# Kernel optimization log

Measured on AMD Instinct MI355X. Metric: run time of the kernel, lower is better.

The kernel has to match this reference:

```python
import jax, jax.numpy as jnp
import numpy as np

PAD = 1
K = 3  # kernel_size


def conv2d(x, w, b):
    y = jax.lax.conv_general_dilated(
        x, w, window_strides=(1, 1), padding=((PAD, PAD), (PAD, PAD)),
        dimension_numbers=("NCHW", "OIHW", "NCHW"))
    return y + b[None, :, None, None]


def deform_conv2d(x, offset, weight, bias):
    # torchvision.ops.deform_conv2d semantics (stride=1, dilation=1, 1 offset group)
    B, C, H, W = x.shape
    O = weight.shape[0]
    K2 = K * K
    off = offset.reshape(B, K2, 2, H, W)  # [...,0]=dy, [...,1]=dx
    ky, kx = jnp.meshgrid(jnp.arange(K), jnp.arange(K), indexing="ij")
    ky = ky.reshape(K2).astype(x.dtype)
    kx = kx.reshape(K2).astype(x.dtype)
    hh = jnp.arange(H, dtype=x.dtype)
    ww = jnp.arange(W, dtype=x.dtype)
    # sampling coords, shape [B, K2, H, W]
    py = off[:, :, 0] + ky[None, :, None, None] + hh[None, None, :, None] - PAD
    px = off[:, :, 1] + kx[None, :, None, None] + ww[None, None, None, :] - PAD

    y0 = jnp.floor(py)
    x0 = jnp.floor(px)
    wy = (py - y0)[:, None]  # [B,1,K2,H,W]
    wx = (px - x0)[:, None]

    xf = x.reshape(B, C, H * W)

    def gather(iy, ix):
        valid = (iy >= 0) & (iy < H) & (ix >= 0) & (ix < W)
        iyc = jnp.clip(iy, 0, H - 1).astype(jnp.int32)
        ixc = jnp.clip(ix, 0, W - 1).astype(jnp.int32)
        idx = (iyc * W + ixc).reshape(B, 1, K2 * H * W)
        v = jnp.take_along_axis(xf, idx, axis=2).reshape(B, C, K2, H, W)
        return v * valid.reshape(B, 1, K2, H, W).astype(x.dtype)

    v00 = gather(y0, x0)
    v01 = gather(y0, x0 + 1)
    v10 = gather(y0 + 1, x0)
    v11 = gather(y0 + 1, x0 + 1)
    sampled = (v00 * (1 - wy) * (1 - wx) + v01 * (1 - wy) * wx
               + v10 * wy * (1 - wx) + v11 * wy * wx)  # [B,C,K2,H,W]
    out = jnp.einsum("bckhw,ock->bohw", sampled, weight.reshape(O, C, K2))
    return out + bias[None, :, None, None]


def setup_inputs() -> dict:
    key = jax.random.key(0)
    k1, k2, k3, k4, k5 = jax.random.split(key, 5)
    B, C, H, W = 4, 64, 192, 192
    O = 64
    x = jax.random.normal(k1, (B, C, H, W), dtype=jnp.float32)
    w_off = jax.random.normal(k2, (2 * K * K, C, K, K), dtype=jnp.float32) * 0.05
    b_off = jnp.zeros((2 * K * K,), dtype=jnp.float32)
    w_conv = jax.random.normal(k3, (O, C, K, K), dtype=jnp.float32) * (1.0 / np.sqrt(C * K * K))
    b_conv = jax.random.normal(k4, (O,), dtype=jnp.float32) * 0.01
    return {"x": x, "w_off": w_off, "b_off": b_off, "w_conv": w_conv, "b_conv": b_conv}


def reference(x, w_off, b_off, w_conv, b_conv):
    offset = conv2d(x, w_off, b_off)
    y = deform_conv2d(x, offset, w_conv, b_conv)
    return conv2d(y, w_conv, b_conv)  # module reuses self.conv on deform output
```

## Files before the change

kernel.cpp:

```cpp
#include <hip/hip_runtime.h>

constexpr int B = 4;
constexpr int C = 64;
constexpr int O = 64;
constexpr int OOFF = 18;
constexpr int H = 192;
constexpr int W = 192;

typedef __attribute__((ext_vector_type(8))) short short8;
typedef __attribute__((ext_vector_type(4))) float float4v;
typedef __attribute__((ext_vector_type(2))) float f32x2;
typedef __attribute__((ext_vector_type(2))) uint u32x2;
typedef __attribute__((ext_vector_type(2))) __bf16 bf16x2;

__device__ inline ushort f2bf(float f) {
  return __builtin_bit_cast(ushort, (__bf16)f);
}
__device__ inline uint pk2bf(float lo, float hi) {
  bf16x2 v;
  v.x = (__bf16)lo;
  v.y = (__bf16)hi;
  return __builtin_bit_cast(uint, v);
}
__device__ inline f32x2 upk(uint u) {
  u32x2 t;
  t.x = u << 16;
  t.y = u & 0xffff0000u;
  return __builtin_bit_cast(f32x2, t);
}

__global__ __launch_bounds__(256) void k_pre(const float* __restrict__ x,
                                             ushort* __restrict__ xtb,
                                             const float* __restrict__ w_conv,
                                             ushort* __restrict__ wBf,
                                             const float* __restrict__ w_off,
                                             ushort* __restrict__ wOf) {
  __shared__ float tile[64][17];
  const int bid = blockIdx.x;
  const int tid = threadIdx.x;
  if (bid < 9216) {
    const int w0 = (bid % 12) * 16;
    const int h = (bid / 12) % 192;
    const int b = bid / 2304;
    const int wl = tid & 15;
    const int c0 = tid >> 4;
#pragma unroll
    for (int r = 0; r < 4; ++r) {
      const int c = c0 + r * 16;
      tile[c][wl] = x[(((size_t)b * C + c) * H + h) * W + w0 + wl];
    }
    __syncthreads();
    const int c = tid & 63;
    const int qq = tid >> 6;
#pragma unroll
    for (int r = 0; r < 4; ++r) {
      const int wq = qq + r * 4;
      xtb[(((size_t)b * H + h) * W + w0 + wq) * C + c] = f2bf(tile[c][wq]);
    }
  } else if (bid < 9360) {
    const int i = (bid - 9216) * 256 + tid;
    const int j = i & 7;
    const int lane = (i >> 3) & 63;
    const int nt = (i >> 9) & 3;
    const int kstep = (i >> 11) & 1;
    const int kk = i >> 12;
    const int n = nt + 4 * (lane & 15);
    const int c = kstep * 32 + ((lane >> 4) & 3) * 8 + j;
    wBf[i] = f2bf(w_conv[((size_t)n * C + c) * 9 + kk]);
  } else {
    const int i = (bid - 9360) * 256 + tid;
    const int j = i & 7;
    const int lane = (i >> 3) & 63;
    const int nt = (i >> 9) & 1;
    const int ks = (i >> 10) & 1;
    const int kk = i >> 11;
    const int n = nt * 16 + (lane & 15);
    const int c = ks * 32 + ((lane >> 4) & 3) * 8 + j;
    wOf[i] = (n < OOFF) ? f2bf(w_off[((size_t)n * C + c) * 9 + kk]) : (ushort)0;
  }
}

__global__ __launch_bounds__(256) void k_fused(
    const ushort* __restrict__ xtb, const ushort* __restrict__ wOf,
    const float* __restrict__ b_off, const ushort* __restrict__ wBf,
    const float* __restrict__ b_conv, ushort* __restrict__ yt) {
  __shared__ ushort sA[4][2][64][8];
  __shared__ __align__(16) float offBuf[4][16][20];

  const int bid = blockIdx.x;
  const int xcd = bid & 7;
  const int s = bid >> 3;
  const int b = xcd >> 1;
  const int half = xcd & 1;
  const int th = half * 12 + s / 24;
  const int tw = s % 24;
  const int h0 = th * 8, w0 = tw * 8;

  const int tid = threadIdx.x;
  const int wave = tid >> 6, lane = tid & 63;
  const int col = lane & 15, quad = lane >> 4;
  const int p = tid >> 2, qtr = tid & 3;
  const int pl = p & 15;
  const int prow = p >> 3, pcol = p & 7;
  const int h = h0 + prow, w = w0 + pcol;
  const int ks_w = qtr >> 1;
  const int q2 = (qtr & 1) * 2;

  {
    float4v oacc[2];
#pragma unroll
    for (int nt = 0; nt < 2; ++nt) oacc[nt] = (float4v){0.f, 0.f, 0.f, 0.f};

    short8 obfr[2][2][2];
    short8 oafr[2][2];

    auto oload = [&](int kk, int pb) {
      const int ky = kk / 3, kx = kk % 3;
      const int hh = h0 + 2 * wave + (col >> 3) + ky - 1;
      const int ww = w0 + (col & 7) + kx - 1;
      const bool ok = ((unsigned)hh < (unsigned)H) && ((unsigned)ww < (unsigned)W);
      const int hhc = min(max(hh, 0), H - 1);
      const int wwc = min(max(ww, 0), W - 1);
      const ushort* pa = xtb + (((size_t)b * H + hhc) * W + wwc) * C + quad * 8;
#pragma unroll
      for (int ks = 0; ks < 2; ++ks) {
        short8 v = (short8)0;
        if (ok) v = *(const short8*)(pa + ks * 32);
        oafr[pb][ks] = v;
#pragma unroll
        for (int nt = 0; nt < 2; ++nt)
          obfr[pb][ks][nt] = *(const short8*)&wOf[((((size_t)kk * 2 + ks) * 2 + nt) * 64 + lane) * 8];
      }
    };

    oload(0, 0);
#pragma unroll
    for (int kk = 0; kk < 9; ++kk) {
      const int pb = kk & 1;
      if (kk < 8) oload(kk + 1, pb ^ 1);
#pragma unroll
      for (int ks = 0; ks < 2; ++ks)
#pragma unroll
        for (int nt = 0; nt < 2; ++nt)
          oacc[nt] = __builtin_amdgcn_mfma_f32_16x16x32_bf16(oafr[pb][ks], obfr[pb][ks][nt],
                                                             oacc[nt], 0, 0, 0);
    }

#pragma unroll
    for (int nt = 0; nt < 2; ++nt) {
      const int oc = nt * 16 + col;
      if (oc < OOFF) {
        const float bias = b_off[oc];
#pragma unroll
        for (int r = 0; r < 4; ++r)
          offBuf[wave][quad * 4 + r][oc] = oacc[nt][r] + bias;
      }
    }
  }

  const ushort* xb = xtb + (size_t)b * H * W * C + qtr * 16;

  uint4 G[2][8];
  float4 aw[2];

  auto issue = [&](int kk, int buf) {
    const float2 ov = *(const float2*)&offBuf[wave][pl][2 * kk];
    const float dy = ov.x, dx = ov.y;
    const int ky = kk / 3, kx = kk % 3;
    const float pyf = dy + (float)(ky + h - 1);
    const float pxf = dx + (float)(kx + w - 1);
    const float fy0 = floorf(pyf), fx0 = floorf(pxf);
    const float wy = pyf - fy0, wx = pxf - fx0;
    const int iy0 = (int)fy0, ix0 = (int)fx0;
    const int iy1 = iy0 + 1, ix1 = ix0 + 1;
    const bool vy0 = (unsigned)iy0 < (unsigned)H;
    const bool vy1 = (unsigned)iy1 < (unsigned)H;
    const bool vx0 = (unsigned)ix0 < (unsigned)W;
    const bool vx1 = (unsigned)ix1 < (unsigned)W;
    aw[buf].x = (vy0 && vx0) ? (1.f - wy) * (1.f - wx) : 0.f;
    aw[buf].y = (vy0 && vx1) ? (1.f - wy) * wx : 0.f;
    aw[buf].z = (vy1 && vx0) ? wy * (1.f - wx) : 0.f;
    aw[buf].w = (vy1 && vx1) ? wy * wx : 0.f;
    const int cy0 = min(max(iy0, 0), H - 1), cy1 = min(max(iy1, 0), H - 1);
    const int cx0 = min(max(ix0, 0), W - 1), cx1 = min(max(ix1, 0), W - 1);
    const uint4* p00 = (const uint4*)(xb + ((size_t)cy0 * W + cx0) * C);
    const uint4* p01 = (const uint4*)(xb + ((size_t)cy0 * W + cx1) * C);
    const uint4* p10 = (const uint4*)(xb + ((size_t)cy1 * W + cx0) * C);
    const uint4* p11 = (const uint4*)(xb + ((size_t)cy1 * W + cx1) * C);
    G[buf][0] = p00[0]; G[buf][1] = p00[1];
    G[buf][2] = p01[0]; G[buf][3] = p01[1];
    G[buf][4] = p10[0]; G[buf][5] = p10[1];
    G[buf][6] = p11[0]; G[buf][7] = p11[1];
  };

  float4v acc[4];
#pragma unroll
  for (int nt = 0; nt < 4; ++nt) acc[nt] = (float4v){0.f, 0.f, 0.f, 0.f};

  issue(0, 0);
#pragma unroll
  for (int kk = 0; kk < 9; ++kk) {
    const int buf = kk & 1;
    if (kk < 8) issue(kk + 1, buf ^ 1);

    const f32x2 a00 = {aw[buf].x, aw[buf].x};
    const f32x2 a01 = {aw[buf].y, aw[buf].y};
    const f32x2 a10 = {aw[buf].z, aw[buf].z};
    const f32x2 a11 = {aw[buf].w, aw[buf].w};
    uint pk[8];
#pragma unroll
    for (int i = 0; i < 8; ++i) {
      const uint u00 = ((const uint*)&G[buf][0])[i];
      const uint u01 = ((const uint*)&G[buf][2])[i];
      const uint u10 = ((const uint*)&G[buf][4])[i];
      const uint u11 = ((const uint*)&G[buf][6])[i];
      f32x2 sv = upk(u00) * a00 + upk(u01) * a01 + upk(u10) * a10 + upk(u11) * a11;
      pk[i] = pk2bf(sv.x, sv.y);
    }
    *(uint4*)&sA[wave][ks_w][pl | (q2 << 4)][0] = *(const uint4*)&pk[0];
    *(uint4*)&sA[wave][ks_w][pl | ((q2 + 1) << 4)][0] = *(const uint4*)&pk[4];

#pragma unroll
    for (int ks = 0; ks < 2; ++ks) {
      const short8 a = *(const short8*)&sA[wave][ks][lane][0];
#pragma unroll
      for (int nt = 0; nt < 4; ++nt) {
        const short8 bb = *(const short8*)&wBf[((((size_t)kk * 2 + ks) * 4 + nt) * 64 + lane) * 8];
        acc[nt] = __builtin_amdgcn_mfma_f32_16x16x32_bf16(a, bb, acc[nt], 0, 0, 0);
      }
    }
  }

  float bias[4];
#pragma unroll
  for (int nt = 0; nt < 4; ++nt) bias[nt] = b_conv[4 * col + nt];
#pragma unroll
  for (int r = 0; r < 4; ++r) {
    const int pp = wave * 16 + quad * 4 + r;
    const int hrow = h0 + (pp >> 3), wcol = w0 + (pp & 7);
    uint2 u;
    u.x = pk2bf(acc[0][r] + bias[0], acc[1][r] + bias[1]);
    u.y = pk2bf(acc[2][r] + bias[2], acc[3][r] + bias[3]);
    *(uint2*)&yt[((size_t)(b * H + hrow) * W + wcol) * C + 4 * col] = u;
  }
}

__global__ __launch_bounds__(256) void k_conv_main_mfma(
    const ushort* __restrict__ yt, const ushort* __restrict__ wBf,
    const float* __restrict__ b_conv, float* __restrict__ out) {
  const int w0 = blockIdx.x * 16;
  const int b = blockIdx.z;
  const int tid = threadIdx.x;
  const int wave = tid >> 6, lane = tid & 63;
  const int col = lane & 15, quad = lane >> 4;
  const int h0 = blockIdx.y * 8 + wave * 2;

  float4v acc[2][4];
#pragma unroll
  for (int mt = 0; mt < 2; ++mt)
#pragma unroll
    for (int nt = 0; nt < 4; ++nt) acc[mt][nt] = (float4v){0.f, 0.f, 0.f, 0.f};

  short8 bfr[2][2][4];
  short8 afr[2][2][2];

  auto load = [&](int kk, int pb) {
    const int ky = kk / 3, kx = kk % 3;
    const int ww = w0 + col + kx - 1;
    const bool wok = (unsigned)ww < (unsigned)W;
    const int wwc = min(max(ww, 0), W - 1);
#pragma unroll
    for (int ks = 0; ks < 2; ++ks)
#pragma unroll
      for (int nt = 0; nt < 4; ++nt)
        bfr[pb][ks][nt] = *(const short8*)&wBf[((((size_t)kk * 2 + ks) * 4 + nt) * 64 + lane) * 8];
#pragma unroll
    for (int mt = 0; mt < 2; ++mt) {
      const int hh = h0 + mt + ky - 1;
      const bool ok = wok && ((unsigned)hh < (unsigned)H);
      const int hhc = min(max(hh, 0), H - 1);
      const ushort* pa = yt + (((size_t)b * H + hhc) * W + wwc) * C + quad * 8;
#pragma unroll
      for (int ks = 0; ks < 2; ++ks) {
        short8 v = (short8)0;
        if (ok) v = *(const short8*)(pa + ks * 32);
        afr[pb][mt][ks] = v;
      }
    }
  };

  load(0, 0);
#pragma unroll
  for (int kk = 0; kk < 9; ++kk) {
    const int pb = kk & 1;
    if (kk < 8) load(kk + 1, pb ^ 1);
#pragma unroll
    for (int ks = 0; ks < 2; ++ks)
#pragma unroll
      for (int mt = 0; mt < 2; ++mt)
#pragma unroll
        for (int nt = 0; nt < 4; ++nt)
          acc[mt][nt] = __builtin_amdgcn_mfma_f32_16x16x32_bf16(afr[pb][mt][ks], bfr[pb][ks][nt],
                                                                acc[mt][nt], 0, 0, 0);
  }

  float bias[4];
#pragma unroll
  for (int nt = 0; nt < 4; ++nt) bias[nt] = b_conv[4 * col + nt];
#pragma unroll
  for (int mt = 0; mt < 2; ++mt) {
    const int h = h0 + mt;
#pragma unroll
    for (int nt = 0; nt < 4; ++nt) {
      const int oc = 4 * col + nt;
      float4 v;
      v.x = acc[mt][nt][0] + bias[nt];
      v.y = acc[mt][nt][1] + bias[nt];
      v.z = acc[mt][nt][2] + bias[nt];
      v.w = acc[mt][nt][3] + bias[nt];
      *(float4*)&out[(((size_t)b * O + oc) * H + h) * W + w0 + quad * 4] = v;
    }
  }
}

extern "C" void kernel_launch(void* const* d_in, const int* in_sizes, int n_in,
                              void* d_out, int out_size, void* d_ws, size_t ws_size,
                              hipStream_t stream) {
  const float* x = (const float*)d_in[0];
  const float* w_off = (const float*)d_in[1];
  const float* b_off = (const float*)d_in[2];
  const float* w_conv = (const float*)d_in[3];
  const float* b_conv = (const float*)d_in[4];
  float* out = (float*)d_out;

  ushort* xtb = (ushort*)d_ws;
  ushort* yt = xtb + (size_t)B * H * W * C;
  ushort* wBf = yt + (size_t)B * H * W * C;
  ushort* wOf = wBf + 36864;

  const dim3 blk(256);
  k_pre<<<dim3(9432), blk, 0, stream>>>(x, xtb, w_conv, wBf, w_off, wOf);
  k_fused<<<dim3(2304), blk, 0, stream>>>(xtb, wOf, b_off, wBf, b_conv, yt);
  k_conv_main_mfma<<<dim3(W / 16, H / 8, B), blk, 0, stream>>>(yt, wBf, b_conv, out);
}
```

Baseline: 200.6 us.

## Split bilinear gather into half-staged loads to cut registers for higher occupancy

New measurement: 292.9 us. +46.0%, slower.

```diff
diff --git a/kernel.cpp b/kernel.cpp
--- a/kernel.cpp
+++ b/kernel.cpp
@@ -80,7 +80,7 @@
   }
 }
 
-__global__ __launch_bounds__(256) void k_fused(
+__global__ __launch_bounds__(256, 8) void k_fused(
     const ushort* __restrict__ xtb, const ushort* __restrict__ wOf,
     const float* __restrict__ b_off, const ushort* __restrict__ wBf,
     const float* __restrict__ b_conv, ushort* __restrict__ yt) {
@@ -89,11 +89,11 @@
 
   const int bid = blockIdx.x;
   const int xcd = bid & 7;
-  const int s = bid >> 3;
+  const int s0 = bid >> 3;
   const int b = xcd >> 1;
   const int half = xcd & 1;
-  const int th = half * 12 + s / 24;
-  const int tw = s % 24;
+  const int th = half * 12 + s0 / 24;
+  const int tw = s0 % 24;
   const int h0 = th * 8, w0 = tw * 8;
 
   const int tid = threadIdx.x;
@@ -111,7 +111,6 @@
 #pragma unroll
     for (int nt = 0; nt < 2; ++nt) oacc[nt] = (float4v){0.f, 0.f, 0.f, 0.f};
 
-    short8 obfr[2][2][2];
     short8 oafr[2][2];
 
     auto oload = [&](int kk, int pb) {
@@ -127,9 +126,6 @@
         short8 v = (short8)0;
         if (ok) v = *(const short8*)(pa + ks * 32);
         oafr[pb][ks] = v;
-#pragma unroll
-        for (int nt = 0; nt < 2; ++nt)
-          obfr[pb][ks][nt] = *(const short8*)&wOf[((((size_t)kk * 2 + ks) * 2 + nt) * 64 + lane) * 8];
       }
     };
 
@@ -141,9 +137,11 @@
 #pragma unroll
       for (int ks = 0; ks < 2; ++ks)
 #pragma unroll
-        for (int nt = 0; nt < 2; ++nt)
-          oacc[nt] = __builtin_amdgcn_mfma_f32_16x16x32_bf16(oafr[pb][ks], obfr[pb][ks][nt],
-                                                             oacc[nt], 0, 0, 0);
+        for (int nt = 0; nt < 2; ++nt) {
+          const short8 bw =
+              *(const short8*)&wOf[((((size_t)kk * 2 + ks) * 2 + nt) * 64 + lane) * 8];
+          oacc[nt] = __builtin_amdgcn_mfma_f32_16x16x32_bf16(oafr[pb][ks], bw, oacc[nt], 0, 0, 0);
+        }
     }
 
 #pragma unroll
@@ -158,12 +156,14 @@
     }
   }
 
-  const ushort* xb = xtb + (size_t)b * H * W * C + qtr * 16;
-
-  uint4 G[2][8];
-  float4 aw[2];
-
-  auto issue = [&](int kk, int buf) {
+  const ushort* xbase = xtb + (size_t)b * H * W * C;
+  const uint qoff = (uint)qtr * 32u;
+
+  uint offs[2][4];
+  float4 awv[2];
+  uint4 gA[4], gB[4];
+
+  auto calc = [&](int kk, int s) {
     const float2 ov = *(const float2*)&offBuf[wave][pl][2 * kk];
     const float dy = ov.x, dx = ov.y;
     const int ky = kk / 3, kx = kk % 3;
@@ -177,48 +177,60 @@
     const bool vy1 = (unsigned)iy1 < (unsigned)H;
     const bool vx0 = (unsigned)ix0 < (unsigned)W;
     const bool vx1 = (unsigned)ix1 < (unsigned)W;
-    aw[buf].x = (vy0 && vx0) ? (1.f - wy) * (1.f - wx) : 0.f;
-    aw[buf].y = (vy0 && vx1) ? (1.f - wy) * wx : 0.f;
-    aw[buf].z = (vy1 && vx0) ? wy * (1.f - wx) : 0.f;
-    aw[buf].w = (vy1 && vx1) ? wy * wx : 0.f;
+    awv[s].x = (vy0 && vx0) ? (1.f - wy) * (1.f - wx) : 0.f;
+    awv[s].y = (vy0 && vx1) ? (1.f - wy) * wx : 0.f;
+    awv[s].z = (vy1 && vx0) ? wy * (1.f - wx) : 0.f;
+    awv[s].w = (vy1 && vx1) ? wy * wx : 0.f;
     const int cy0 = min(max(iy0, 0), H - 1), cy1 = min(max(iy1, 0), H - 1);
     const int cx0 = min(max(ix0, 0), W - 1), cx1 = min(max(ix1, 0), W - 1);
-    const uint4* p00 = (const uint4*)(xb + ((size_t)cy0 * W + cx0) * C);
-    const uint4* p01 = (const uint4*)(xb + ((size_t)cy0 * W + cx1) * C);
-    const uint4* p10 = (const uint4*)(xb + ((size_t)cy1 * W + cx0) * C);
-    const uint4* p11 = (const uint4*)(xb + ((size_t)cy1 * W + cx1) * C);
-    G[buf][0] = p00[0]; G[buf][1] = p00[1];
-    G[buf][2] = p01[0]; G[buf][3] = p01[1];
-    G[buf][4] = p10[0]; G[buf][5] = p10[1];
-    G[buf][6] = p11[0]; G[buf][7] = p11[1];
+    offs[s][0] = (uint)((cy0 * W + cx0) * (C * 2)) + qoff;
+    offs[s][1] = (uint)((cy0 * W + cx1) * (C * 2)) + qoff;
+    offs[s][2] = (uint)((cy1 * W + cx0) * (C * 2)) + qoff;
+    offs[s][3] = (uint)((cy1 * W + cx1) * (C * 2)) + qoff;
+  };
+
+  auto loadA = [&](int s) {
+#pragma unroll
+    for (int c = 0; c < 4; ++c)
+      gA[c] = *(const uint4*)((const char*)xbase + offs[s][c]);
+  };
+  auto loadB = [&](int s) {
+#pragma unroll
+    for (int c = 0; c < 4; ++c)
+      gB[c] = *(const uint4*)((const char*)xbase + offs[s][c] + 16u);
+  };
+  auto blend = [&](const uint4* g, int s, uint* pk) {
+    const f32x2 a00 = {awv[s].x, awv[s].x};
+    const f32x2 a01 = {awv[s].y, awv[s].y};
+    const f32x2 a10 = {awv[s].z, awv[s].z};
+    const f32x2 a11 = {awv[s].w, awv[s].w};
+#pragma unroll
+    for (int i = 0; i < 4; ++i) {
+      f32x2 sv = upk(g[0][i]) * a00 + upk(g[1][i]) * a01 + upk(g[2][i]) * a10 + upk(g[3][i]) * a11;
+      pk[i] = pk2bf(sv.x, sv.y);
+    }
   };
 
   float4v acc[4];
 #pragma unroll
   for (int nt = 0; nt < 4; ++nt) acc[nt] = (float4v){0.f, 0.f, 0.f, 0.f};
 
-  issue(0, 0);
+  calc(0, 0);
+  loadA(0);
 #pragma unroll
   for (int kk = 0; kk < 9; ++kk) {
-    const int buf = kk & 1;
-    if (kk < 8) issue(kk + 1, buf ^ 1);
-
-    const f32x2 a00 = {aw[buf].x, aw[buf].x};
-    const f32x2 a01 = {aw[buf].y, aw[buf].y};
-    const f32x2 a10 = {aw[buf].z, aw[buf].z};
-    const f32x2 a11 = {aw[buf].w, aw[buf].w};
-    uint pk[8];
-#pragma unroll
-    for (int i = 0; i < 8; ++i) {
-      const uint u00 = ((const uint*)&G[buf][0])[i];
-      const uint u01 = ((const uint*)&G[buf][2])[i];
-      const uint u10 = ((const uint*)&G[buf][4])[i];
-      const uint u11 = ((const uint*)&G[buf][6])[i];
-      f32x2 sv = upk(u00) * a00 + upk(u01) * a01 + upk(u10) * a10 + upk(u11) * a11;
-      pk[i] = pk2bf(sv.x, sv.y);
-    }
-    *(uint4*)&sA[wave][ks_w][pl | (q2 << 4)][0] = *(const uint4*)&pk[0];
-    *(uint4*)&sA[wave][ks_w][pl | ((q2 + 1) << 4)][0] = *(const uint4*)&pk[4];
+    const int s = kk & 1, ns = s ^ 1;
+    loadB(s);
+    if (kk < 8) calc(kk + 1, ns);
+
+    uint pkA[4];
+    blend(gA, s, pkA);
+    *(uint4*)&sA[wave][ks_w][pl | (q2 << 4)][0] = *(const uint4*)pkA;
+    if (kk < 8) loadA(ns);
+
+    uint pkB[4];
+    blend(gB, s, pkB);
+    *(uint4*)&sA[wave][ks_w][pl | ((q2 + 1) << 4)][0] = *(const uint4*)pkB;
 
 #pragma unroll
     for (int ks = 0; ks < 2; ++ks) {
```
